# Performance work log

Hardware: AMD Instinct MI355X
Metric: run time of the kernel (lower is better)

The kernel has to match this reference:

```python
import jax, jax.numpy as jnp
import numpy as np

DT_RANK = 12


def _mixer(x, in_w, conv_w, conv_b, xproj_w, dt_w, dt_b, A_log, D_skip, out_w):
    # x: [B, L, d_model]
    B, L, _ = x.shape
    d_inner, d_state = A_log.shape
    k = conv_w.shape[-1]
    xz = x @ in_w.T                                  # [B, L, 2*d_inner]
    x_part, z = jnp.split(xz, 2, axis=-1)
    # causal depthwise conv1d (torch pads both sides with k-1 then slices [:L] == left-pad only)
    xc = x_part.transpose(0, 2, 1)                   # [B, d_inner, L]
    xc = jax.lax.conv_general_dilated(
        xc, conv_w, window_strides=(1,), padding=[(k - 1, 0)],
        feature_group_count=d_inner, dimension_numbers=("NCH", "OIH", "NCH"))
    xc = xc + conv_b[None, :, None]
    x_part = jax.nn.silu(xc.transpose(0, 2, 1))      # [B, L, d_inner]
    dt_bc = x_part @ xproj_w.T                       # [B, L, dt_rank + 2*d_state]
    dt_part = dt_bc[..., :DT_RANK]
    b_term = jnp.tanh(dt_bc[..., DT_RANK:DT_RANK + d_state])
    c_term = jnp.tanh(dt_bc[..., DT_RANK + d_state:])
    dt = jax.nn.softplus(dt_part @ dt_w.T + dt_b) + 1e-4   # [B, L, d_inner]
    a = -jnp.exp(A_log)                              # [d_inner, d_state]

    def step(state, inp):
        x_t, dt_t, b_t, c_t = inp                    # [B,di], [B,di], [B,N], [B,N]
        da = jnp.exp(dt_t[:, :, None] * a)           # [B, di, N]
        db = (1.0 - da) * b_t[:, None, :]
        state = da * state + db * x_t[:, :, None]
        y_t = (state * c_t[:, None, :]).sum(-1) + D_skip * x_t
        return state, y_t

    init = jnp.zeros((B, d_inner, d_state), x.dtype)
    xs = (x_part.transpose(1, 0, 2), dt.transpose(1, 0, 2),
          b_term.transpose(1, 0, 2), c_term.transpose(1, 0, 2))
    _, ys = jax.lax.scan(step, init, xs)             # ys: [L, B, d_inner]
    y = ys.transpose(1, 0, 2) * jax.nn.silu(z)
    return y @ out_w.T                               # [B, L, d_model]


def setup_inputs() -> dict:
    key = jax.random.key(0)
    B, L, D = 32, 577, 192
    d_inner, d_state, d_conv = 384, 8, 4
    ks = jax.random.split(key, 16)
    s = 0.02
    inp = {"x": jax.random.normal(ks[0], (B, L, D), jnp.float32)}
    for i, p in enumerate(["fw", "bw"]):
        kk = jax.random.split(ks[1 + i], 8)
        inp[f"{p}_in_w"] = jax.random.normal(kk[0], (2 * d_inner, D), jnp.float32) * s
        inp[f"{p}_conv_w"] = jax.random.normal(kk[1], (d_inner, 1, d_conv), jnp.float32) * 0.1
        inp[f"{p}_conv_b"] = jnp.zeros((d_inner,), jnp.float32)
        inp[f"{p}_xproj_w"] = jax.random.normal(kk[2], (DT_RANK + 2 * d_state, d_inner), jnp.float32) * s
        inp[f"{p}_dt_w"] = jax.random.normal(kk[3], (d_inner, DT_RANK), jnp.float32) * s
        inp[f"{p}_dt_b"] = jnp.zeros((d_inner,), jnp.float32)
        inp[f"{p}_A_log"] = jax.random.uniform(kk[4], (d_inner, d_state), jnp.float32)
        inp[f"{p}_D"] = jnp.ones((d_inner,), jnp.float32)
        inp[f"{p}_out_w"] = jax.random.normal(kk[5], (D, d_inner), jnp.float32) * s
    return inp


def reference(x,
              fw_in_w, fw_conv_w, fw_conv_b, fw_xproj_w, fw_dt_w, fw_dt_b, fw_A_log, fw_D, fw_out_w,
              bw_in_w, bw_conv_w, bw_conv_b, bw_xproj_w, bw_dt_w, bw_dt_b, bw_A_log, bw_D, bw_out_w):
    y_fwd = _mixer(x, fw_in_w, fw_conv_w, fw_conv_b, fw_xproj_w, fw_dt_w, fw_dt_b, fw_A_log, fw_D, fw_out_w)
    x_rev = jnp.flip(x, axis=1)
    y_bwd = _mixer(x_rev, bw_in_w, bw_conv_w, bw_conv_b, bw_xproj_w, bw_dt_w, bw_dt_b, bw_A_log, bw_D, bw_out_w)
    y_bwd = jnp.flip(y_bwd, axis=1)
    return 0.5 * (y_fwd + y_bwd)
```

## Files before the change

### kernel.cpp

```cpp
#include <hip/hip_runtime.h>
#include <hip/hip_bf16.h>

#define L2E 1.44269504088896340f
#define LN2 0.69314718055994531f

typedef __bf16 bf16x8 __attribute__((ext_vector_type(8)));
typedef __bf16 bf16x4 __attribute__((ext_vector_type(4)));
typedef float f32x4 __attribute__((ext_vector_type(4)));

__device__ __forceinline__ float fexp2(float x){ return __builtin_amdgcn_exp2f(x); }
__device__ __forceinline__ float flog2(float x){ return __builtin_amdgcn_logf(x); }
__device__ __forceinline__ float frcp(float x){ return __builtin_amdgcn_rcpf(x); }
__device__ __forceinline__ float fsigmoid(float x){ return frcp(1.f + fexp2(-x*L2E)); }
__device__ __forceinline__ float fsoftplus(float x){
  float sp = flog2(1.f + fexp2(x*L2E))*LN2;
  return (x > 15.f) ? x : sp;
}
__device__ __forceinline__ float ftanh_(float x){
  x = fminf(fmaxf(x, -10.f), 10.f);
  float e = fexp2(2.f*L2E*x);
  return (e - 1.f)*frcp(e + 1.f);
}

#define NB 32
#define LS 577
#define DM 192
#define DI 384
#define BL 18464
#define M2T 36928
#define T_CH 37
#define N_CH 16

__global__ __launch_bounds__(256) void k_prep(
    const float* __restrict__ x,
    const float* __restrict__ fw_in, const float* __restrict__ bw_in,
    const float* __restrict__ fw_out, const float* __restrict__ bw_out,
    const float* __restrict__ fw_xp, const float* __restrict__ bw_xp,
    const float* __restrict__ fw_al, const float* __restrict__ bw_al,
    __hip_bfloat16* __restrict__ xbf, __hip_bfloat16* __restrict__ wcat,
    __hip_bfloat16* __restrict__ wout, __hip_bfloat16* __restrict__ xpp,
    float* __restrict__ alog2)
{
  const int S0 = 3545088;
  const int S1 = S0 + 294912;
  const int S2 = S1 + 147456;
  const int S3 = S2 + 24576;
  const int S4 = S3 + 6144;
  int idx = blockIdx.x*256 + threadIdx.x;
  if (idx < S0) {
    xbf[idx] = __float2bfloat16(x[idx]);
  } else if (idx < S1) {
    int i = idx - S0; int r = i/192, k = i - r*192;
    float v = (r < 768) ? fw_in[r*192+k] : bw_in[(r-768)*192+k];
    wcat[i] = __float2bfloat16(v);
  } else if (idx < S2) {
    int i = idx - S1; int o = i/768, k = i - o*768;
    float v = 0.5f * ((k < 384) ? fw_out[o*384+k] : bw_out[o*384+(k-384)]);
    wout[i] = __float2bfloat16(v);
  } else if (idx < S3) {
    int i = idx - S2; int d = i/12288; int rr = i - d*12288;
    int n = rr/384, k = rr - n*384;
    const float* xp = d ? bw_xp : fw_xp;
    float v = (n < 28) ? xp[n*384+k] : 0.f;
    xpp[i] = __float2bfloat16(v);
  } else if (idx < S4) {
    int i = idx - S3;
    const float* al = (i < 3072) ? fw_al : bw_al;
    int j = (i < 3072) ? i : (i - 3072);
    alog2[i] = -fexp2(al[j]*L2E) * L2E;
  }
}

#define G1_LDA 104
#define G1_LDO 136
__global__ __launch_bounds__(256) void k_gemm1(const __hip_bfloat16* __restrict__ A,
                                               const __hip_bfloat16* __restrict__ Bw,
                                               __hip_bfloat16* __restrict__ xg,
                                               __hip_bfloat16* __restrict__ zsb)
{
  __shared__ __align__(16) __bf16 smem[26624];
  __bf16* ldsA = smem;
  __bf16* ldsB = smem + 128*G1_LDA;

  const int t = threadIdx.x;
  const int tm = blockIdx.x / 12, tn = blockIdx.x - tm*12;
  const int m0 = tm*128, n0 = tn*128;
  const int w = t >> 6, lane = t & 63;
  const int wr = (w >> 1)*64, wc = (w & 1)*64;
  const int r = lane & 15, q = lane >> 4;

  f32x4 acc[4][4];
  #pragma unroll
  for (int a=0;a<4;++a)
    #pragma unroll
    for (int b=0;b<4;++b) acc[a][b] = (f32x4){0.f,0.f,0.f,0.f};

  #pragma unroll
  for (int h=0; h<2; ++h) {
    if (h) __syncthreads();
    #pragma unroll
    for (int j=0;j<6;++j) {
      int cid = t + 256*j;
      int row = cid/12; int c8 = (cid - row*12)*8;
      int gr = m0 + row; if (gr > BL-1) gr = BL-1;
      bf16x8 va = *(const bf16x8*)(A + (size_t)gr*192 + h*96 + c8);
      *(bf16x8*)(ldsA + row*G1_LDA + c8) = va;
      bf16x8 vb = *(const bf16x8*)(Bw + (size_t)(n0+row)*192 + h*96 + c8);
      *(bf16x8*)(ldsB + row*G1_LDA + c8) = vb;
    }
    __syncthreads();
    #pragma unroll
    for (int kc=0; kc<96; kc+=32) {
      bf16x8 af[4], bfv[4];
      #pragma unroll
      for (int mi=0; mi<4; ++mi)
        af[mi] = *(const bf16x8*)(ldsA + (wr + mi*16 + r)*G1_LDA + q*8 + kc);
      #pragma unroll
      for (int ni=0; ni<4; ++ni)
        bfv[ni] = *(const bf16x8*)(ldsB + (wc + ni*16 + r)*G1_LDA + q*8 + kc);
      #pragma unroll
      for (int mi=0; mi<4; ++mi)
        #pragma unroll
        for (int ni=0; ni<4; ++ni)
          acc[mi][ni] = __builtin_amdgcn_mfma_f32_16x16x32_bf16(af[mi], bfv[ni], acc[mi][ni], 0,0,0);
    }
  }

  const int cat = tn/3;
  const int cbase = (tn - cat*3)*128;
  const int d = cat >> 1, isz = cat & 1;
  __syncthreads();
  __bf16* ldsO = smem;
  #pragma unroll
  for (int mi=0; mi<4; ++mi)
    #pragma unroll
    for (int ni=0; ni<4; ++ni)
      #pragma unroll
      for (int rg=0; rg<4; ++rg) {
        int row = wr + mi*16 + q*4 + rg;
        int col = wc + ni*16 + r;
        float v = acc[mi][ni][rg];
        if (isz) v = v * fsigmoid(v);
        ldsO[row*G1_LDO + col] = (__bf16)v;
      }
  __syncthreads();
  __hip_bfloat16* dst = (isz ? zsb : xg) + (size_t)(d*BL)*384 + cbase;
  const int c8 = (t & 15)*8;
  #pragma unroll
  for (int it=0; it<8; ++it) {
    int row = (t >> 4) + it*16;
    int grow = m0 + row;
    if (grow < BL) {
      bf16x8 v = *(const bf16x8*)(ldsO + row*G1_LDO + c8);
      *(bf16x8*)(dst + (size_t)grow*384 + c8) = v;
    }
  }
}

__global__ __launch_bounds__(256) void k_conv(const __hip_bfloat16* __restrict__ xg,
                                              __hip_bfloat16* __restrict__ xcs,
                                              const float* __restrict__ fw_cw, const float* __restrict__ fw_cb,
                                              const float* __restrict__ bw_cw, const float* __restrict__ bw_cb)
{
  int idx = blockIdx.x*256 + threadIdx.x;
  int token = idx / 96; int g = idx - token*96; int c0 = g*4;
  int d = token / BL; int r2 = token - d*BL;
  int b = r2 / LS; int i = r2 - b*LS;
  const float* cwp = (d ? bw_cw : fw_cw);
  const float* cbp = (d ? bw_cb : fw_cb);
  f32x4 w0 = *(const f32x4*)(cwp + (c0+0)*4);
  f32x4 w1 = *(const f32x4*)(cwp + (c0+1)*4);
  f32x4 w2 = *(const f32x4*)(cwp + (c0+2)*4);
  f32x4 w3 = *(const f32x4*)(cwp + (c0+3)*4);
  f32x4 accv = *(const f32x4*)(cbp + c0);
  const __hip_bfloat16* base = xg + ((size_t)(d*BL + b*LS))*384 + c0;
  #pragma unroll
  for (int j=0;j<4;++j) {
    int iw = d ? (i+3-j) : (i-3+j);
    bool valid = d ? (iw < LS) : (iw >= 0);
    if (valid) {
      bf16x4 xv = *(const bf16x4*)(base + (size_t)iw*384);
      f32x4 wj = (f32x4){w0[j], w1[j], w2[j], w3[j]};
      #pragma unroll
      for (int ch=0; ch<4; ++ch) accv[ch] += wj[ch]*(float)xv[ch];
    }
  }
  bf16x4 outv;
  #pragma unroll
  for (int ch=0; ch<4; ++ch) {
    float s = accv[ch]*fsigmoid(accv[ch]);
    outv[ch] = (__bf16)s;
  }
  *(bf16x4*)(xcs + (size_t)token*384 + c0) = outv;
}

__global__ __launch_bounds__(256) void k_dtbc(const __hip_bfloat16* __restrict__ A,
                                              const __hip_bfloat16* __restrict__ xpp,
                                              float* __restrict__ dtbc)
{
  const int wid = blockIdx.x*4 + (threadIdx.x >> 6);
  if (wid >= 1154) return;
  const int lane = threadIdx.x & 63;
  const int m0 = wid*32;
  const int r = lane & 15, q = lane >> 4;
  const int d = (m0 >= BL) ? 1 : 0;
  const __hip_bfloat16* Bp = xpp + (size_t)d*32*384;
  f32x4 acc[2][2];
  #pragma unroll
  for (int a=0;a<2;++a)
    #pragma unroll
    for (int b=0;b<2;++b) acc[a][b] = (f32x4){0.f,0.f,0.f,0.f};
  const __hip_bfloat16* Ab = A + (size_t)(m0 + r)*384 + q*8;
  const __hip_bfloat16* Bb = Bp + (size_t)r*384 + q*8;
  #pragma unroll
  for (int kc = 0; kc < 384; kc += 32) {
    bf16x8 af0 = *(const bf16x8*)(Ab + kc);
    bf16x8 af1 = *(const bf16x8*)(Ab + 16*384 + kc);
    bf16x8 bf0 = *(const bf16x8*)(Bb + kc);
    bf16x8 bf1 = *(const bf16x8*)(Bb + 16*384 + kc);
    acc[0][0] = __builtin_amdgcn_mfma_f32_16x16x32_bf16(af0, bf0, acc[0][0], 0,0,0);
    acc[0][1] = __builtin_amdgcn_mfma_f32_16x16x32_bf16(af0, bf1, acc[0][1], 0,0,0);
    acc[1][0] = __builtin_amdgcn_mfma_f32_16x16x32_bf16(af1, bf0, acc[1][0], 0,0,0);
    acc[1][1] = __builtin_amdgcn_mfma_f32_16x16x32_bf16(af1, bf1, acc[1][1], 0,0,0);
  }
  #pragma unroll
  for (int mi=0; mi<2; ++mi)
    #pragma unroll
    for (int ni=0; ni<2; ++ni)
      #pragma unroll
      for (int rg=0; rg<4; ++rg) {
        int n = ni*16 + r;
        if (n < 28) {
          int m = m0 + mi*16 + q*4 + rg;
          float v = acc[mi][ni][rg];
          if (n >= 12) v = ftanh_(v);
          int r2 = m - d*BL; int b = r2 / LS; int i = r2 - b*LS;
          int ts = d ? (LS-1-i) : i;
          dtbc[((size_t)((d*NB + b)*LS + ts))*28 + n] = v;
        }
      }
}

__global__ __launch_bounds__(256) void k_dtfull(const float* __restrict__ dtbc,
                                                const float* __restrict__ fw_dtw, const float* __restrict__ fw_dtb,
                                                const float* __restrict__ bw_dtw, const float* __restrict__ bw_dtb,
                                                float* __restrict__ dtf)
{
  int idx = blockIdx.x*256 + threadIdx.x;
  int m = idx / 96; int g = idx - m*96; int c0 = g*4;
  int d = (m >= BL) ? 1 : 0;
  const float* dtw = (d ? bw_dtw : fw_dtw);
  const float* dtbp = (d ? bw_dtb : fw_dtb);
  const float* dp = dtbc + (size_t)m*28;
  f32x4 p0 = *(const f32x4*)(dp);
  f32x4 p1 = *(const f32x4*)(dp+4);
  f32x4 p2 = *(const f32x4*)(dp+8);
  f32x4 acc = *(const f32x4*)(dtbp + c0);
  #pragma unroll
  for (int ch=0; ch<4; ++ch) {
    const float* wv = dtw + (size_t)(c0+ch)*12;
    f32x4 w0 = *(const f32x4*)(wv);
    f32x4 w1 = *(const f32x4*)(wv+4);
    f32x4 w2 = *(const f32x4*)(wv+8);
    float s = acc[ch];
    #pragma unroll
    for (int r=0;r<4;++r) s += p0[r]*w0[r];
    #pragma unroll
    for (int r=0;r<4;++r) s += p1[r]*w1[r];
    #pragma unroll
    for (int r=0;r<4;++r) s += p2[r]*w2[r];
    acc[ch] = fsoftplus(s) + 1e-4f;
  }
  *(f32x4*)(dtf + (size_t)m*384 + c0) = acc;
}

__global__ __launch_bounds__(64) void k_scan1(const __hip_bfloat16* __restrict__ xcs,
                                              const float* __restrict__ dtbc,
                                              const float* __restrict__ dtf,
                                              const float* __restrict__ alog2,
                                              float* __restrict__ ps)
{
  __shared__ __align__(16) float sB[T_CH*8];
  const int bid = blockIdx.x;
  const int lane = threadIdx.x;
  const int kc = bid & 15; const int dbc = bid >> 4;
  const int cchunk = dbc % 6; const int db = dbc / 6;
  const int b = db & 31; const int d = db >> 5;
  const int c = cchunk*64 + lane;

  const int ts0 = kc*T_CH;
  const int ts1 = (ts0 + T_CH < LS) ? (ts0 + T_CH) : LS;

  {
    const float* src = dtbc + ((size_t)((d*NB+b)*LS + ts0))*28;
    int n4 = (ts1 - ts0)*2;
    for (int j = lane; j < n4; j += 64)
      *(f32x4*)(sB + j*4) = *(const f32x4*)(src + (size_t)(j>>1)*28 + 12 + (j&1)*4);
  }

  float al[8];
  const float* alp = alog2 + ((size_t)(d*384 + c))*8;
  #pragma unroll
  for (int s=0;s<8;++s) al[s] = alp[s];

  const __hip_bfloat16* xcb = xcs + ((size_t)(d*BL + b*LS))*384 + c;
  const float* dfb = dtf + ((size_t)((d*NB+b)*LS))*384 + c;

  float P[8], S[8];
  #pragma unroll
  for (int s=0;s<8;++s){ P[s]=1.f; S[s]=0.f; }

  __syncthreads();

  float xnb, dtn;
  {
    int i = d ? (LS-1-ts0) : ts0;
    xnb = __bfloat162float(xcb[(size_t)i*384]);
    dtn = dfb[(size_t)ts0*384];
  }
  for (int ts=ts0; ts<ts1; ++ts) {
    f32x4 B0 = *(const f32x4*)(sB + (ts-ts0)*8);
    f32x4 B1 = *(const f32x4*)(sB + (ts-ts0)*8 + 4);
    float xt = xnb, dt = dtn;
    if (ts+1 < ts1) {
      int i2 = d ? (LS-2-ts) : (ts+1);
      xnb = __bfloat162float(xcb[(size_t)i2*384]);
      dtn = dfb[(size_t)(ts+1)*384];
    }
    #pragma unroll
    for (int s=0;s<8;++s) {
      float da = fexp2(dt * al[s]);
      float Bv = (s<4) ? B0[s] : B1[s-4];
      float tmp = Bv*xt;
      S[s] = tmp + da*(S[s]-tmp);
      P[s] *= da;
    }
  }
  float* pp = ps + ((size_t)bid*16)*64 + lane;
  #pragma unroll
  for (int s=0;s<8;++s) pp[s*64] = P[s];
  #pragma unroll
  for (int s=0;s<8;++s) pp[(8+s)*64] = S[s];
}

__global__ __launch_bounds__(64) void k_comb(const float* __restrict__ ps,
                                             float* __restrict__ initst)
{
  const int dbc = blockIdx.x;
  const int lane = threadIdx.x;
  float st[8];
  #pragma unroll
  for (int s=0;s<8;++s) st[s]=0.f;
  for (int kc=0;kc<N_CH;++kc) {
    const float* pp = ps + ((size_t)(dbc*N_CH+kc)*16)*64 + lane;
    float* ip = initst + ((size_t)(dbc*N_CH+kc)*8)*64 + lane;
    #pragma unroll
    for (int s=0;s<8;++s) ip[s*64] = st[s];
    #pragma unroll
    for (int s=0;s<8;++s) {
      float P = pp[s*64], Sv = pp[(8+s)*64];
      st[s] = P*st[s] + Sv;
    }
  }
}

__global__ __launch_bounds__(64) void k_scan2(const __hip_bfloat16* __restrict__ xcs,
                                              const __hip_bfloat16* __restrict__ zsb,
                                              const float* __restrict__ dtbc,
                                              const float* __restrict__ dtf,
                                              const float* __restrict__ initst,
                                              const float* __restrict__ fw_D,
                                              const float* __restrict__ bw_D,
                                              const float* __restrict__ alog2,
                                              __hip_bfloat16* __restrict__ ybf)
{
  __shared__ __align__(16) float sBC[T_CH*16];
  const int bid = blockIdx.x;
  const int lane = threadIdx.x;
  const int kc = bid & 15; const int dbc = bid >> 4;
  const int cchunk = dbc % 6; const int db = dbc / 6;
  const int b = db & 31; const int d = db >> 5;
  const int c = cchunk*64 + lane;

  const int ts0 = kc*T_CH;
  const int ts1 = (ts0 + T_CH < LS) ? (ts0 + T_CH) : LS;

  {
    const float* src = dtbc + ((size_t)((d*NB+b)*LS + ts0))*28;
    int n4 = (ts1 - ts0)*4;
    for (int j = lane; j < n4; j += 64)
      *(f32x4*)(sBC + j*4) = *(const f32x4*)(src + (size_t)(j>>2)*28 + 12 + (j&3)*4);
  }

  const float Dc  = (d ? bw_D : fw_D)[c];
  float al[8];
  const float* alp = alog2 + ((size_t)(d*384 + c))*8;
  #pragma unroll
  for (int s=0;s<8;++s) al[s] = alp[s];

  float st[8];
  {
    const float* ip = initst + ((size_t)bid*8)*64 + lane;
    #pragma unroll
    for (int s=0;s<8;++s) st[s] = ip[s*64];
  }

  const __hip_bfloat16* xcb = xcs + ((size_t)(d*BL + b*LS))*384 + c;
  const __hip_bfloat16* zcb = zsb + ((size_t)(d*BL + b*LS))*384 + c;
  const float* dfb = dtf + ((size_t)((d*NB+b)*LS))*384 + c;
  __hip_bfloat16* ybase = ybf + (size_t)(b*LS)*768 + d*384 + c;

  __syncthreads();

  float xnb, znb, dtn;
  {
    int i = d ? (LS-1-ts0) : ts0;
    xnb = __bfloat162float(xcb[(size_t)i*384]);
    znb = __bfloat162float(zcb[(size_t)i*384]);
    dtn = dfb[(size_t)ts0*384];
  }
  for (int ts=ts0; ts<ts1; ++ts) {
    f32x4 B0 = *(const f32x4*)(sBC + (ts-ts0)*16);
    f32x4 B1 = *(const f32x4*)(sBC + (ts-ts0)*16 + 4);
    f32x4 C0 = *(const f32x4*)(sBC + (ts-ts0)*16 + 8);
    f32x4 C1 = *(const f32x4*)(sBC + (ts-ts0)*16 + 12);
    float xt = xnb, zs = znb, dt = dtn;
    int i = d ? (LS-1-ts) : ts;
    if (ts+1 < ts1) {
      int i2 = d ? (LS-2-ts) : (ts+1);
      xnb = __bfloat162float(xcb[(size_t)i2*384]);
      znb = __bfloat162float(zcb[(size_t)i2*384]);
      dtn = dfb[(size_t)(ts+1)*384];
    }
    float y = Dc * xt;
    #pragma unroll
    for (int s=0;s<8;++s) {
      float da = fexp2(dt * al[s]);
      float Bv = (s<4) ? B0[s] : B1[s-4];
      float Cv = (s<4) ? C0[s] : C1[s-4];
      float tmp = Bv*xt;
      st[s] = tmp + da*(st[s]-tmp);
      y += st[s]*Cv;
    }
    ybase[(size_t)i*768] = __float2bfloat16(y*zs);
  }
}

#define G2_LDA 104
__global__ __launch_bounds__(256) void k_gemm2(const __hip_bfloat16* __restrict__ A,
                                               const __hip_bfloat16* __restrict__ Bw,
                                               float* __restrict__ C)
{
  __shared__ __align__(16) __bf16 smem[26624];
  __bf16* ldsA = smem;
  __bf16* ldsB = smem + 64*G2_LDA;

  const int t = threadIdx.x;
  const int m0 = blockIdx.x*64;
  const int w = t >> 6, lane = t & 63;
  const int wr = (w >> 1)*32, wc = (w & 1)*96;
  const int r = lane & 15, q = lane >> 4;

  f32x4 acc[2][6];
  #pragma unroll
  for (int a=0;a<2;++a)
    #pragma unroll
    for (int b=0;b<6;++b) acc[a][b] = (f32x4){0.f,0.f,0.f,0.f};

  #pragma unroll 1
  for (int h=0; h<8; ++h) {
    if (h) __syncthreads();
    #pragma unroll
    for (int j=0;j<3;++j) {
      int cid = t + 256*j;
      int row = cid/12; int c8 = (cid - row*12)*8;
      int gr = m0 + row; if (gr > BL-1) gr = BL-1;
      *(bf16x8*)(ldsA + row*G2_LDA + c8) = *(const bf16x8*)(A + (size_t)gr*768 + h*96 + c8);
    }
    #pragma unroll
    for (int j=0;j<9;++j) {
      int cid = t + 256*j;
      int row = cid/12; int c8 = (cid - row*12)*8;
      *(bf16x8*)(ldsB + row*G2_LDA + c8) = *(const bf16x8*)(Bw + (size_t)row*768 + h*96 + c8);
    }
    __syncthreads();
    #pragma unroll
    for (int kc=0; kc<96; kc+=32) {
      bf16x8 af[2], bfv[6];
      #pragma unroll
      for (int mi=0; mi<2; ++mi)
        af[mi] = *(const bf16x8*)(ldsA + (wr + mi*16 + r)*G2_LDA + q*8 + kc);
      #pragma unroll
      for (int ni=0; ni<6; ++ni)
        bfv[ni] = *(const bf16x8*)(ldsB + (wc + ni*16 + r)*G2_LDA + q*8 + kc);
      #pragma unroll
      for (int mi=0; mi<2; ++mi)
        #pragma unroll
        for (int ni=0; ni<6; ++ni)
          acc[mi][ni] = __builtin_amdgcn_mfma_f32_16x16x32_bf16(af[mi], bfv[ni], acc[mi][ni], 0,0,0);
    }
  }

  #pragma unroll
  for (int mi=0; mi<2; ++mi)
    #pragma unroll
    for (int ni=0; ni<6; ++ni)
      #pragma unroll
      for (int rg=0; rg<4; ++rg) {
        int row = m0 + wr + mi*16 + q*4 + rg;
        int col = wc + ni*16 + r;
        if (row < BL) C[(size_t)row*192 + col] = acc[mi][ni][rg];
      }
}

extern "C" void kernel_launch(void* const* d_in, const int* in_sizes, int n_in,
                              void* d_out, int out_size, void* d_ws, size_t ws_size,
                              hipStream_t stream) {
  const float* x        = (const float*)d_in[0];
  const float* fw_in_w  = (const float*)d_in[1];
  const float* fw_cw    = (const float*)d_in[2];
  const float* fw_cb    = (const float*)d_in[3];
  const float* fw_xp    = (const float*)d_in[4];
  const float* fw_dtw   = (const float*)d_in[5];
  const float* fw_dtb   = (const float*)d_in[6];
  const float* fw_al    = (const float*)d_in[7];
  const float* fw_D     = (const float*)d_in[8];
  const float* fw_ow    = (const float*)d_in[9];
  const float* bw_in_w  = (const float*)d_in[10];
  const float* bw_cw    = (const float*)d_in[11];
  const float* bw_cb    = (const float*)d_in[12];
  const float* bw_xp    = (const float*)d_in[13];
  const float* bw_dtw   = (const float*)d_in[14];
  const float* bw_dtb   = (const float*)d_in[15];
  const float* bw_al    = (const float*)d_in[16];
  const float* bw_D     = (const float*)d_in[17];
  const float* bw_ow    = (const float*)d_in[18];

  char* ws = (char*)d_ws;
  __hip_bfloat16* wcat = (__hip_bfloat16*)(ws + 0);
  __hip_bfloat16* wout = (__hip_bfloat16*)(ws + 589824);
  __hip_bfloat16* xpp  = (__hip_bfloat16*)(ws + 884736);
  float* alog2         = (float*)(ws + 933888);
  __hip_bfloat16* xbf  = (__hip_bfloat16*)(ws + 958464);
  __hip_bfloat16* xg   = (__hip_bfloat16*)(ws + 8048640);
  float* initst        = (float*)(ws + 8048640);
  __hip_bfloat16* zsb  = (__hip_bfloat16*)(ws + 36409344);
  __hip_bfloat16* xcs  = (__hip_bfloat16*)(ws + 64770048);
  float* dtbc          = (float*)(ws + 93130752);
  float* dtf           = (float*)(ws + 97266688);
  float* ps            = (float*)(ws + 153988096);
  __hip_bfloat16* ybf  = (__hip_bfloat16*)(ws + 153988096);

  hipLaunchKernelGGL(k_prep, dim3(15696), dim3(256), 0, stream,
                     x, fw_in_w, bw_in_w, fw_ow, bw_ow, fw_xp, bw_xp, fw_al, bw_al,
                     xbf, wcat, wout, xpp, alog2);
  hipLaunchKernelGGL(k_gemm1, dim3(1740), dim3(256), 0, stream, xbf, wcat, xg, zsb);
  hipLaunchKernelGGL(k_conv, dim3(13848), dim3(256), 0, stream,
                     xg, xcs, fw_cw, fw_cb, bw_cw, bw_cb);
  hipLaunchKernelGGL(k_dtbc, dim3(289), dim3(256), 0, stream, xcs, xpp, dtbc);
  hipLaunchKernelGGL(k_dtfull, dim3(13848), dim3(256), 0, stream,
                     dtbc, fw_dtw, fw_dtb, bw_dtw, bw_dtb, dtf);
  hipLaunchKernelGGL(k_scan1, dim3(6144), dim3(64), 0, stream,
                     xcs, dtbc, dtf, alog2, ps);
  hipLaunchKernelGGL(k_comb, dim3(384), dim3(64), 0, stream, ps, initst);
  hipLaunchKernelGGL(k_scan2, dim3(6144), dim3(64), 0, stream,
                     xcs, zsb, dtbc, dtf, initst, fw_D, bw_D, alog2, ybf);
  hipLaunchKernelGGL(k_gemm2, dim3(289), dim3(256), 0, stream, ybf, wout, (float*)d_out);
}
```

Measured before the change: 308.9 us.

## Store dt in fp16 and fold chunk-state combine into second scan pass

The per-channel dt tensor is written and read as fp16 instead of fp32, halving its memory traffic in k_dtfull, k_scan1 and k_scan2. The separate k_comb kernel is removed, and each k_scan2 block now rebuilds its initial state by sequentially combining the prefix chunk summaries itself, which saves a launch and the initst round trip. The trade-offs are redundant prefix work (up to 15 chunk reads per block), reduced dt precision, and a rearranged workspace layout where ybf now reuses the xg region.

```diff
diff --git a/kernel.cpp b/kernel.cpp
--- a/kernel.cpp
+++ b/kernel.cpp
@@ -7,6 +7,7 @@
 typedef __bf16 bf16x8 __attribute__((ext_vector_type(8)));
 typedef __bf16 bf16x4 __attribute__((ext_vector_type(4)));
 typedef float f32x4 __attribute__((ext_vector_type(4)));
+typedef _Float16 h16x4 __attribute__((ext_vector_type(4)));
 
 __device__ __forceinline__ float fexp2(float x){ return __builtin_amdgcn_exp2f(x); }
 __device__ __forceinline__ float flog2(float x){ return __builtin_amdgcn_logf(x); }
@@ -244,7 +245,7 @@
 __global__ __launch_bounds__(256) void k_dtfull(const float* __restrict__ dtbc,
                                                 const float* __restrict__ fw_dtw, const float* __restrict__ fw_dtb,
                                                 const float* __restrict__ bw_dtw, const float* __restrict__ bw_dtb,
-                                                float* __restrict__ dtf)
+                                                _Float16* __restrict__ dtf)
 {
   int idx = blockIdx.x*256 + threadIdx.x;
   int m = idx / 96; int g = idx - m*96; int c0 = g*4;
@@ -256,6 +257,7 @@
   f32x4 p1 = *(const f32x4*)(dp+4);
   f32x4 p2 = *(const f32x4*)(dp+8);
   f32x4 acc = *(const f32x4*)(dtbp + c0);
+  h16x4 o;
   #pragma unroll
   for (int ch=0; ch<4; ++ch) {
     const float* wv = dtw + (size_t)(c0+ch)*12;
@@ -269,14 +271,14 @@
     for (int r=0;r<4;++r) s += p1[r]*w1[r];
     #pragma unroll
     for (int r=0;r<4;++r) s += p2[r]*w2[r];
-    acc[ch] = fsoftplus(s) + 1e-4f;
-  }
-  *(f32x4*)(dtf + (size_t)m*384 + c0) = acc;
+    o[ch] = (_Float16)(fsoftplus(s) + 1e-4f);
+  }
+  *(h16x4*)(dtf + (size_t)m*384 + c0) = o;
 }
 
 __global__ __launch_bounds__(64) void k_scan1(const __hip_bfloat16* __restrict__ xcs,
                                               const float* __restrict__ dtbc,
-                                              const float* __restrict__ dtf,
+                                              const _Float16* __restrict__ dtf,
                                               const float* __restrict__ alog2,
                                               float* __restrict__ ps)
 {
@@ -304,7 +306,7 @@
   for (int s=0;s<8;++s) al[s] = alp[s];
 
   const __hip_bfloat16* xcb = xcs + ((size_t)(d*BL + b*LS))*384 + c;
-  const float* dfb = dtf + ((size_t)((d*NB+b)*LS))*384 + c;
+  const _Float16* dfb = dtf + ((size_t)((d*NB+b)*LS))*384 + c;
 
   float P[8], S[8];
   #pragma unroll
@@ -316,7 +318,7 @@
   {
     int i = d ? (LS-1-ts0) : ts0;
     xnb = __bfloat162float(xcb[(size_t)i*384]);
-    dtn = dfb[(size_t)ts0*384];
+    dtn = (float)dfb[(size_t)ts0*384];
   }
   for (int ts=ts0; ts<ts1; ++ts) {
     f32x4 B0 = *(const f32x4*)(sB + (ts-ts0)*8);
@@ -325,7 +327,7 @@
     if (ts+1 < ts1) {
       int i2 = d ? (LS-2-ts) : (ts+1);
       xnb = __bfloat162float(xcb[(size_t)i2*384]);
-      dtn = dfb[(size_t)(ts+1)*384];
+      dtn = (float)dfb[(size_t)(ts+1)*384];
     }
     #pragma unroll
     for (int s=0;s<8;++s) {
@@ -343,32 +345,11 @@
   for (int s=0;s<8;++s) pp[(8+s)*64] = S[s];
 }
 
-__global__ __launch_bounds__(64) void k_comb(const float* __restrict__ ps,
-                                             float* __restrict__ initst)
-{
-  const int dbc = blockIdx.x;
-  const int lane = threadIdx.x;
-  float st[8];
-  #pragma unroll
-  for (int s=0;s<8;++s) st[s]=0.f;
-  for (int kc=0;kc<N_CH;++kc) {
-    const float* pp = ps + ((size_t)(dbc*N_CH+kc)*16)*64 + lane;
-    float* ip = initst + ((size_t)(dbc*N_CH+kc)*8)*64 + lane;
-    #pragma unroll
-    for (int s=0;s<8;++s) ip[s*64] = st[s];
-    #pragma unroll
-    for (int s=0;s<8;++s) {
-      float P = pp[s*64], Sv = pp[(8+s)*64];
-      st[s] = P*st[s] + Sv;
-    }
-  }
-}
-
 __global__ __launch_bounds__(64) void k_scan2(const __hip_bfloat16* __restrict__ xcs,
                                               const __hip_bfloat16* __restrict__ zsb,
                                               const float* __restrict__ dtbc,
-                                              const float* __restrict__ dtf,
-                                              const float* __restrict__ initst,
+                                              const _Float16* __restrict__ dtf,
+                                              const float* __restrict__ ps,
                                               const float* __restrict__ fw_D,
                                               const float* __restrict__ bw_D,
                                               const float* __restrict__ alog2,
@@ -399,15 +380,22 @@
   for (int s=0;s<8;++s) al[s] = alp[s];
 
   float st[8];
-  {
-    const float* ip = initst + ((size_t)bid*8)*64 + lane;
-    #pragma unroll
-    for (int s=0;s<8;++s) st[s] = ip[s*64];
+  #pragma unroll
+  for (int s=0;s<8;++s) st[s] = 0.f;
+  for (int j=0; j<kc; ++j) {
+    const float* pp = ps + ((size_t)(dbc*16+j)*16)*64 + lane;
+    float Pj[8], Sj[8];
+    #pragma unroll
+    for (int s=0;s<8;++s) Pj[s] = pp[s*64];
+    #pragma unroll
+    for (int s=0;s<8;++s) Sj[s] = pp[(8+s)*64];
+    #pragma unroll
+    for (int s=0;s<8;++s) st[s] = Pj[s]*st[s] + Sj[s];
   }
 
   const __hip_bfloat16* xcb = xcs + ((size_t)(d*BL + b*LS))*384 + c;
   const __hip_bfloat16* zcb = zsb + ((size_t)(d*BL + b*LS))*384 + c;
-  const float* dfb = dtf + ((size_t)((d*NB+b)*LS))*384 + c;
+  const _Float16* dfb = dtf + ((size_t)((d*NB+b)*LS))*384 + c;
   __hip_bfloat16* ybase = ybf + (size_t)(b*LS)*768 + d*384 + c;
 
   __syncthreads();
@@ -417,7 +405,7 @@
     int i = d ? (LS-1-ts0) : ts0;
     xnb = __bfloat162float(xcb[(size_t)i*384]);
     znb = __bfloat162float(zcb[(size_t)i*384]);
-    dtn = dfb[(size_t)ts0*384];
+    dtn = (float)dfb[(size_t)ts0*384];
   }
   for (int ts=ts0; ts<ts1; ++ts) {
     f32x4 B0 = *(const f32x4*)(sBC + (ts-ts0)*16);
@@ -430,7 +418,7 @@
       int i2 = d ? (LS-2-ts) : (ts+1);
       xnb = __bfloat162float(xcb[(size_t)i2*384]);
       znb = __bfloat162float(zcb[(size_t)i2*384]);
-      dtn = dfb[(size_t)(ts+1)*384];
+      dtn = (float)dfb[(size_t)(ts+1)*384];
     }
     float y = Dc * xt;
     #pragma unroll
@@ -543,13 +531,12 @@
   float* alog2         = (float*)(ws + 933888);
   __hip_bfloat16* xbf  = (__hip_bfloat16*)(ws + 958464);
   __hip_bfloat16* xg   = (__hip_bfloat16*)(ws + 8048640);
-  float* initst        = (float*)(ws + 8048640);
+  __hip_bfloat16* ybf  = (__hip_bfloat16*)(ws + 8048640);
   __hip_bfloat16* zsb  = (__hip_bfloat16*)(ws + 36409344);
   __hip_bfloat16* xcs  = (__hip_bfloat16*)(ws + 64770048);
   float* dtbc          = (float*)(ws + 93130752);
-  float* dtf           = (float*)(ws + 97266688);
-  float* ps            = (float*)(ws + 153988096);
-  __hip_bfloat16* ybf  = (__hip_bfloat16*)(ws + 153988096);
+  _Float16* dtf        = (_Float16*)(ws + 97266688);
+  float* ps            = (float*)(ws + 125627392);
 
   hipLaunchKernelGGL(k_prep, dim3(15696), dim3(256), 0, stream,
                      x, fw_in_w, bw_in_w, fw_ow, bw_ow, fw_xp, bw_xp, fw_al, bw_al,
@@ -562,8 +549,7 @@
                      dtbc, fw_dtw, fw_dtb, bw_dtw, bw_dtb, dtf);
   hipLaunchKernelGGL(k_scan1, dim3(6144), dim3(64), 0, stream,
                      xcs, dtbc, dtf, alog2, ps);
-  hipLaunchKernelGGL(k_comb, dim3(384), dim3(64), 0, stream, ps, initst);
   hipLaunchKernelGGL(k_scan2, dim3(6144), dim3(64), 0, stream,
-                     xcs, zsb, dtbc, dtf, initst, fw_D, bw_D, alog2, ybf);
+                     xcs, zsb, dtbc, dtf, ps, fw_D, bw_D, alog2, ybf);
   hipLaunchKernelGGL(k_gemm2, dim3(289), dim3(256), 0, stream, ybf, wout, (float*)d_out);
 }
```

Measured after the change: 330.5 us. 7.0% more time.
